# Kernel tuning notes

Hardware: AMD Instinct MI355X
Metric: run time of the kernel (lower is better)

The kernel has to match this reference:

```python
import jax, jax.numpy as jnp
import numpy as np

N = 50000   # nodes
E = 600000  # edges (avg degree 12)
D = 128     # feature dim (input_dim == output_dim for residual)
G = 8       # graphs in batch
EPS = 1e-5


def setup_inputs() -> dict:
    key = jax.random.key(0)
    ks = jax.random.split(key, 8)
    x = jax.random.normal(ks[0], (N, D), dtype=jnp.float32)
    edge_index = jax.random.randint(ks[1], (2, E), 0, N)
    batch = jnp.sort(jax.random.randint(ks[2], (N,), 0, G))
    s = 1.0 / np.sqrt(D)
    Wl = jax.random.normal(ks[3], (D, D), dtype=jnp.float32) * s
    bl = jax.random.normal(ks[4], (D,), dtype=jnp.float32) * s
    Wr = jax.random.normal(ks[5], (D, D), dtype=jnp.float32) * s
    return {
        "x": x,
        "edge_index": edge_index,
        "batch": batch,
        "num_graphs": G,
        "Wl": Wl,
        "bl": bl,
        "Wr": Wr,
        "gn_weight": jnp.ones((D,), jnp.float32),
        "gn_bias": jnp.zeros((D,), jnp.float32),
        "mean_scale": jnp.ones((D,), jnp.float32),
    }


def reference(x, edge_index, batch, num_graphs, Wl, bl, Wr, gn_weight, gn_bias, mean_scale):
    n = x.shape[0]
    src, dst = edge_index[0], edge_index[1]

    # SAGEConv: mean-aggregate neighbor (source) features at target nodes
    ones_e = jnp.ones(src.shape[0], dtype=x.dtype)
    deg = jax.ops.segment_sum(ones_e, dst, num_segments=n)          # [N]
    agg = jax.ops.segment_sum(x[src], dst, num_segments=n)          # [N, D]
    agg = agg / jnp.maximum(deg, 1.0)[:, None]
    f = agg @ Wl.T + bl + x @ Wr.T                                  # lin_l(agg) + lin_r(x)

    # exact (erf) GELU, as torch F.gelu default
    f = jax.nn.gelu(f, approximate=False)

    # GraphNorm: per-graph statistics with learnable mean_scale
    ones_n = jnp.ones(n, dtype=x.dtype)
    cnt = jax.ops.segment_sum(ones_n, batch, num_segments=num_graphs)[:, None]  # [G,1]
    mean = jax.ops.segment_sum(f, batch, num_segments=num_graphs) / cnt         # [G,D]
    out = f - mean_scale * mean[batch]
    var = jax.ops.segment_sum(out * out, batch, num_segments=num_graphs) / cnt  # [G,D]
    out = out / jnp.sqrt(var[batch] + EPS) * gn_weight + gn_bias

    # dropout is identity in eval mode; residual add
    return out + x
```

## Files before the change

### kernel.cpp

```cpp
#include <hip/hip_runtime.h>

#define D 128
#define NGRAPH 8
#define EPS 1e-5f
#define CAP 48

typedef __attribute__((ext_vector_type(4))) float f32x4;
typedef __attribute__((ext_vector_type(8))) short s16x8;

__device__ __forceinline__ unsigned short f2bf(float f) {
    unsigned int u = __float_as_uint(f);
    u += 0x7fffu + ((u >> 16) & 1u);
    return (unsigned short)(u >> 16);
}
__device__ __forceinline__ float blo(unsigned int u) { return __uint_as_float(u << 16); }
__device__ __forceinline__ float bhi(unsigned int u) { return __uint_as_float(u & 0xffff0000u); }

__global__ __launch_bounds__(256) void prep_fill_kernel(
    const float* __restrict__ Wl, const float* __restrict__ Wr,
    unsigned short* __restrict__ Bsw,
    const float* __restrict__ x, unsigned int* __restrict__ xb,
    const int* __restrict__ batch, int* __restrict__ bnd,
    const int* __restrict__ ei, int* __restrict__ cnt, int* __restrict__ adj,
    int N, int E, int Npad, int fillB)
{
    int b = blockIdx.x;
    if (b < 128) {
        int t = b * 256 + threadIdx.x;
        int j    = t & 7;
        int ln   = (t >> 3) & 63;
        int ks   = (t >> 9) & 7;
        int tile = t >> 12;
        int k = ks * 32 + (ln >> 4) * 8 + j;
        int d = tile * 16 + (ln & 15);
        float v = (k < 128) ? Wl[(size_t)d * 128 + k] : Wr[(size_t)d * 128 + (k - 128)];
        Bsw[t] = f2bf(v);
    } else if (b == 128) {
        int g = threadIdx.x;
        if (g <= NGRAPH) {
            int lo = 0, hi = N;
            while (lo < hi) {
                int mid = (lo + hi) >> 1;
                if (batch[mid] < g) lo = mid + 1; else hi = mid;
            }
            bnd[g] = lo;
        }
    } else if (b < 129 + fillB) {
        int e = (b - 129) * 256 + threadIdx.x;
        if (e < E) {
            int dst = ei[E + e];
            int pos = atomicAdd(&cnt[dst], 1);
            if (pos < CAP) adj[(size_t)dst * CAP + pos] = ei[e];
        }
    } else {
        int iu = (b - 129 - fillB) * 256 + threadIdx.x;
        if (iu < N * 32) {
            float4 p = *(const float4*)(x + (size_t)iu * 4);
            uint2 o;
            o.x = (unsigned int)f2bf(p.x) | ((unsigned int)f2bf(p.y) << 16);
            o.y = (unsigned int)f2bf(p.z) | ((unsigned int)f2bf(p.w) << 16);
            *(uint2*)(xb + (size_t)iu * 2) = o;
        } else if (iu < Npad * 32) {
            *(uint2*)(xb + (size_t)iu * 2) = make_uint2(0u, 0u);
        }
    }
}

__global__ __launch_bounds__(256) void aggregate_kernel(
    const unsigned int* __restrict__ xb, const int* __restrict__ cnt,
    const int* __restrict__ adj, unsigned int* __restrict__ Aag, int N, int Npad)
{
    int n = blockIdx.x * 4 + (threadIdx.x >> 6);
    int lane = threadIdx.x & 63;
    if (n >= Npad) return;
    if (n >= N) { Aag[(size_t)n * 64 + lane] = 0u; return; }
    int deg = cnt[n];
    int lim = deg < CAP ? deg : CAP;
    int v = (lane < lim) ? adj[(size_t)n * CAP + lane] : 0;
    float a0 = 0.0f, a1 = 0.0f;
    int i = 0;
    for (; i + 8 <= lim; i += 8) {
        int nb[8];
#pragma unroll
        for (int k = 0; k < 8; ++k) nb[k] = __shfl(v, i + k, 64);
        unsigned int u[8];
#pragma unroll
        for (int k = 0; k < 8; ++k) u[k] = xb[(size_t)nb[k] * 64 + lane];
#pragma unroll
        for (int k = 0; k < 8; ++k) { a0 += blo(u[k]); a1 += bhi(u[k]); }
    }
    for (; i < lim; ++i) {
        int nb = __shfl(v, i, 64);
        unsigned int u = xb[(size_t)nb * 64 + lane];
        a0 += blo(u); a1 += bhi(u);
    }
    float inv = 1.0f / (float)(deg > 0 ? deg : 1);
    Aag[(size_t)n * 64 + lane] =
        (unsigned int)f2bf(a0 * inv) | ((unsigned int)f2bf(a1 * inv) << 16);
}

template<int COOP>
__global__ __launch_bounds__(256, 4) void fused_kernel(
    const unsigned short* __restrict__ Aag, const unsigned short* __restrict__ xb16,
    const unsigned short* __restrict__ Bsw, const float* __restrict__ bl,
    const int* __restrict__ batch, const int* __restrict__ bnd,
    const float* __restrict__ x,
    const float* __restrict__ ms, const float* __restrict__ gw,
    const float* __restrict__ gb,
    float* __restrict__ gsum, float* __restrict__ gsumsq,
    unsigned int* __restrict__ bar, float* __restrict__ fout,
    float* __restrict__ out, int N)
{
    int wave = threadIdx.x >> 6, lane = threadIdx.x & 63;
    int row0 = blockIdx.x * 64 + wave * 16;
    int m = lane & 15, quad = lane >> 4;
    int r = row0 + m;

    s16x8 afrag[8];
    const unsigned short* ab = Aag + (size_t)r * 128 + quad * 8;
#pragma unroll
    for (int ks = 0; ks < 4; ++ks) afrag[ks] = *(const s16x8*)(ab + ks * 32);
    const unsigned short* xp = xb16 + (size_t)r * 128 + quad * 8;
#pragma unroll
    for (int ks = 0; ks < 4; ++ks) afrag[4 + ks] = *(const s16x8*)(xp + ks * 32);

    int nbase = row0;
    bool uni = (nbase + 15 < N) && (batch[nbase] == batch[nbase + 15]);
    int gu = (nbase < N) ? batch[nbase] : 0;

    float val[8][4];
#pragma unroll
    for (int tile = 0; tile < 8; ++tile) {
        f32x4 acc = {0.0f, 0.0f, 0.0f, 0.0f};
        const s16x8* bptr = (const s16x8*)Bsw + (size_t)(tile * 8) * 64 + lane;
#pragma unroll
        for (int ks = 0; ks < 8; ++ks)
            acc = __builtin_amdgcn_mfma_f32_16x16x32_bf16(afrag[ks], bptr[(size_t)ks * 64], acc, 0, 0, 0);
        int d = tile * 16 + m;
        float bias = bl[d];
        float sm = 0.0f, sq = 0.0f;
#pragma unroll
        for (int rr = 0; rr < 4; ++rr) {
            int node = nbase + quad * 4 + rr;
            float v = acc[rr] + bias;
            float g = 0.5f * v * (1.0f + erff(v * 0.70710678118654752f));
            val[tile][rr] = g;
            if (node < N) {
                if (uni) { sm += g; sq += g * g; }
                else {
                    int gg = batch[node];
                    unsafeAtomicAdd(&gsum[gg * D + d], g);
                    unsafeAtomicAdd(&gsumsq[gg * D + d], g * g);
                }
            }
        }
        if (uni) {
            sm += __shfl_xor(sm, 16, 64); sm += __shfl_xor(sm, 32, 64);
            sq += __shfl_xor(sq, 16, 64); sq += __shfl_xor(sq, 32, 64);
            if (quad == 0) {
                unsafeAtomicAdd(&gsum[gu * D + d], sm);
                unsafeAtomicAdd(&gsumsq[gu * D + d], sq);
            }
        }
    }

    if constexpr (!COOP) {
#pragma unroll
        for (int tile = 0; tile < 8; ++tile) {
            int d = tile * 16 + m;
#pragma unroll
            for (int rr = 0; rr < 4; ++rr) {
                int node = nbase + quad * 4 + rr;
                if (node < N) fout[(size_t)node * D + d] = val[tile][rr];
            }
        }
        return;
    }

    __syncthreads();
    if (threadIdx.x == 0) {
        __hip_atomic_fetch_add(bar, 1u, __ATOMIC_ACQ_REL, __HIP_MEMORY_SCOPE_AGENT);
        unsigned long long t0 = __builtin_amdgcn_s_memrealtime();
        while (__hip_atomic_load(bar, __ATOMIC_RELAXED, __HIP_MEMORY_SCOPE_AGENT) < gridDim.x) {
            __builtin_amdgcn_s_sleep(10);
            if (__builtin_amdgcn_s_memrealtime() - t0 > 5000000ull) break;
        }
    }
    __syncthreads();

    int node0 = nbase + quad * 4;
    if (node0 < N) {
        int last = (node0 + 3 < N - 1) ? node0 + 3 : N - 1;
        int g0 = batch[node0];
        int gL = batch[last];
        if (g0 == gL) {
            int c = bnd[g0 + 1] - bnd[g0];
            float invc = 1.0f / (float)(c > 0 ? c : 1);
#pragma unroll
            for (int tile = 0; tile < 8; ++tile) {
                int d = tile * 16 + m;
                float s1 = __hip_atomic_load(&gsum[g0 * D + d], __ATOMIC_RELAXED, __HIP_MEMORY_SCOPE_AGENT);
                float s2 = __hip_atomic_load(&gsumsq[g0 * D + d], __ATOMIC_RELAXED, __HIP_MEMORY_SCOPE_AGENT);
                float mu = s1 * invc, q = s2 * invc, a = ms[d] * mu;
                float sc = rsqrtf(q - 2.0f * a * mu + a * a + EPS);
                float gwv = gw[d], gbv = gb[d];
#pragma unroll
                for (int rr = 0; rr < 4; ++rr) {
                    int node = node0 + rr;
                    if (node < N)
                        out[(size_t)node * D + d] =
                            (val[tile][rr] - a) * sc * gwv + gbv + x[(size_t)node * D + d];
                }
            }
        } else {
#pragma unroll
            for (int rr = 0; rr < 4; ++rr) {
                int node = node0 + rr;
                if (node >= N) continue;
                int g = batch[node];
                int c = bnd[g + 1] - bnd[g];
                float invc = 1.0f / (float)(c > 0 ? c : 1);
#pragma unroll
                for (int tile = 0; tile < 8; ++tile) {
                    int d = tile * 16 + m;
                    float s1 = __hip_atomic_load(&gsum[g * D + d], __ATOMIC_RELAXED, __HIP_MEMORY_SCOPE_AGENT);
                    float s2 = __hip_atomic_load(&gsumsq[g * D + d], __ATOMIC_RELAXED, __HIP_MEMORY_SCOPE_AGENT);
                    float mu = s1 * invc, q = s2 * invc, a = ms[d] * mu;
                    float sc = rsqrtf(q - 2.0f * a * mu + a * a + EPS);
                    out[(size_t)node * D + d] =
                        (val[tile][rr] - a) * sc * gw[d] + gb[d] + x[(size_t)node * D + d];
                }
            }
        }
    }
}

__global__ __launch_bounds__(256) void final_kernel(
    const float* __restrict__ f, const float* __restrict__ x,
    const int* __restrict__ batch, const int* __restrict__ bnd,
    const float* __restrict__ gsum, const float* __restrict__ gsumsq,
    const float* __restrict__ ms,
    const float* __restrict__ gw, const float* __restrict__ gb,
    float* __restrict__ out, int N)
{
    int t = blockIdx.x * 256 + threadIdx.x;
    if (t >= N * (D / 4)) return;
    int n  = t >> 5;
    int d0 = (t & 31) * 4;
    int g  = batch[n];
    int c  = bnd[g + 1] - bnd[g];
    float invc = 1.0f / (float)(c > 0 ? c : 1);
    size_t row = (size_t)n * D + d0;
    float4 fv = *(const float4*)(f + row);
    float4 xv = *(const float4*)(x + row);
    float4 s1 = *(const float4*)(gsum + g * D + d0);
    float4 s2 = *(const float4*)(gsumsq + g * D + d0);
    float4 msv = *(const float4*)(ms + d0);
    float4 gwv = *(const float4*)(gw + d0);
    float4 gbv = *(const float4*)(gb + d0);
    float4 o;
    {
        float mu = s1.x * invc, q = s2.x * invc, a = msv.x * mu;
        float sc = rsqrtf(q - 2.0f * a * mu + a * a + EPS);
        o.x = (fv.x - a) * sc * gwv.x + gbv.x + xv.x;
    }
    {
        float mu = s1.y * invc, q = s2.y * invc, a = msv.y * mu;
        float sc = rsqrtf(q - 2.0f * a * mu + a * a + EPS);
        o.y = (fv.y - a) * sc * gwv.y + gbv.y + xv.y;
    }
    {
        float mu = s1.z * invc, q = s2.z * invc, a = msv.z * mu;
        float sc = rsqrtf(q - 2.0f * a * mu + a * a + EPS);
        o.z = (fv.z - a) * sc * gwv.z + gbv.z + xv.z;
    }
    {
        float mu = s1.w * invc, q = s2.w * invc, a = msv.w * mu;
        float sc = rsqrtf(q - 2.0f * a * mu + a * a + EPS);
        o.w = (fv.w - a) * sc * gwv.w + gbv.w + xv.w;
    }
    *(float4*)(out + row) = o;
}

extern "C" void kernel_launch(void* const* d_in, const int* in_sizes, int n_in,
                              void* d_out, int out_size, void* d_ws, size_t ws_size,
                              hipStream_t stream)
{
    const float* x     = (const float*)d_in[0];
    const int*   ei    = (const int*)d_in[1];
    const int*   batch = (const int*)d_in[2];
    const float* Wl = (const float*)d_in[4];
    const float* bl = (const float*)d_in[5];
    const float* Wr = (const float*)d_in[6];
    const float* gw = (const float*)d_in[7];
    const float* gb = (const float*)d_in[8];
    const float* ms = (const float*)d_in[9];
    float* out = (float*)d_out;

    int N = in_sizes[0] / D;
    int E = in_sizes[1] / 2;
    int NBLK = (N + 63) / 64;
    int Npad = NBLK * 64;

    float*          fout = (float*)d_ws;
    unsigned int*   xb   = (unsigned int*)(fout + (size_t)Npad * D);
    unsigned short* Bsw  = (unsigned short*)(xb + (size_t)Npad * 64);
    float* gsum   = (float*)(Bsw + 32768);
    float* gsumsq = gsum + NGRAPH * D;
    unsigned int* bar = (unsigned int*)(gsumsq + NGRAPH * D);
    int*   cnt    = (int*)(bar + 4);
    int*   bnd    = cnt + N;
    int*   adj    = bnd + (NGRAPH + 1);
    unsigned int* Aag = (unsigned int*)(adj + (size_t)N * CAP);

    hipMemsetAsync(gsum, 0,
                   (2 * NGRAPH * D) * sizeof(float) + 4 * sizeof(unsigned int)
                   + (size_t)N * sizeof(int), stream);

    int fillB = (E + 255) / 256;
    int xbB   = (Npad * 32 + 255) / 256;
    prep_fill_kernel<<<129 + fillB + xbB, 256, 0, stream>>>(
        Wl, Wr, Bsw, x, xb, batch, bnd, ei, cnt, adj, N, E, Npad, fillB);

    aggregate_kernel<<<Npad / 4, 256, 0, stream>>>(xb, cnt, adj, Aag, N, Npad);

    int occ = 0, ncu = 0, dev = 0;
    bool coop = false;
    if (hipOccupancyMaxActiveBlocksPerMultiprocessor(&occ, fused_kernel<1>, 256, 0) == hipSuccess) {
        if (hipGetDevice(&dev) != hipSuccess) dev = 0;
        if (hipDeviceGetAttribute(&ncu, hipDeviceAttributeMultiprocessorCount, dev) != hipSuccess || ncu <= 0)
            ncu = 256;
        coop = ((long long)occ * (long long)ncu >= (long long)NBLK);
    }

    if (coop) {
        fused_kernel<1><<<NBLK, 256, 0, stream>>>(
            (const unsigned short*)Aag, (const unsigned short*)xb, Bsw, bl,
            batch, bnd, x, ms, gw, gb, gsum, gsumsq, bar, fout, out, N);
    } else {
        fused_kernel<0><<<NBLK, 256, 0, stream>>>(
            (const unsigned short*)Aag, (const unsigned short*)xb, Bsw, bl,
            batch, bnd, x, ms, gw, gb, gsum, gsumsq, bar, fout, out, N);
        int threads = N * (D / 4);
        final_kernel<<<(threads + 255) / 256, 256, 0, stream>>>(
            fout, x, batch, bnd, gsum, gsumsq, ms, gw, gb, out, N);
    }
}
```

Before: 203.7 us.

## Gather neighbors from fp8 copy and split output columns across waves

```diff
diff --git a/kernel.cpp b/kernel.cpp
--- a/kernel.cpp
+++ b/kernel.cpp
@@ -6,6 +6,7 @@
 #define CAP 48
 
 typedef __attribute__((ext_vector_type(4))) float f32x4;
+typedef __attribute__((ext_vector_type(2))) float f32x2;
 typedef __attribute__((ext_vector_type(8))) short s16x8;
 
 __device__ __forceinline__ unsigned short f2bf(float f) {
@@ -20,6 +21,7 @@
     const float* __restrict__ Wl, const float* __restrict__ Wr,
     unsigned short* __restrict__ Bsw,
     const float* __restrict__ x, unsigned int* __restrict__ xb,
+    unsigned int* __restrict__ xf8,
     const int* __restrict__ batch, int* __restrict__ bnd,
     const int* __restrict__ ei, int* __restrict__ cnt, int* __restrict__ adj,
     int N, int E, int Npad, int fillB)
@@ -54,20 +56,27 @@
         }
     } else {
         int iu = (b - 129 - fillB) * 256 + threadIdx.x;
-        if (iu < N * 32) {
-            float4 p = *(const float4*)(x + (size_t)iu * 4);
-            uint2 o;
-            o.x = (unsigned int)f2bf(p.x) | ((unsigned int)f2bf(p.y) << 16);
-            o.y = (unsigned int)f2bf(p.z) | ((unsigned int)f2bf(p.w) << 16);
-            *(uint2*)(xb + (size_t)iu * 2) = o;
-        } else if (iu < Npad * 32) {
-            *(uint2*)(xb + (size_t)iu * 2) = make_uint2(0u, 0u);
+        if (iu < Npad * 32) {
+            int n = iu >> 5, slot = iu & 31;
+            if (iu < N * 32) {
+                float4 p = *(const float4*)(x + (size_t)iu * 4);
+                uint2 o;
+                o.x = (unsigned int)f2bf(p.x) | ((unsigned int)f2bf(p.y) << 16);
+                o.y = (unsigned int)f2bf(p.z) | ((unsigned int)f2bf(p.w) << 16);
+                *(uint2*)(xb + (size_t)iu * 2) = o;
+                int u8 = __builtin_amdgcn_cvt_pk_fp8_f32(p.x, p.y, 0, false);
+                u8     = __builtin_amdgcn_cvt_pk_fp8_f32(p.z, p.w, u8, true);
+                xf8[(size_t)n * 32 + slot] = (unsigned int)u8;
+            } else {
+                *(uint2*)(xb + (size_t)iu * 2) = make_uint2(0u, 0u);
+                xf8[(size_t)n * 32 + slot] = 0u;
+            }
         }
     }
 }
 
 __global__ __launch_bounds__(256) void aggregate_kernel(
-    const unsigned int* __restrict__ xb, const int* __restrict__ cnt,
+    const unsigned short* __restrict__ xf8, const int* __restrict__ cnt,
     const int* __restrict__ adj, unsigned int* __restrict__ Aag, int N, int Npad)
 {
     int n = blockIdx.x * 4 + (threadIdx.x >> 6);
@@ -83,16 +92,20 @@
         int nb[8];
 #pragma unroll
         for (int k = 0; k < 8; ++k) nb[k] = __shfl(v, i + k, 64);
-        unsigned int u[8];
-#pragma unroll
-        for (int k = 0; k < 8; ++k) u[k] = xb[(size_t)nb[k] * 64 + lane];
-#pragma unroll
-        for (int k = 0; k < 8; ++k) { a0 += blo(u[k]); a1 += bhi(u[k]); }
+        unsigned short u[8];
+#pragma unroll
+        for (int k = 0; k < 8; ++k) u[k] = xf8[(size_t)nb[k] * 64 + lane];
+#pragma unroll
+        for (int k = 0; k < 8; ++k) {
+            f32x2 d2 = __builtin_amdgcn_cvt_pk_f32_fp8((int)(unsigned int)u[k], false);
+            a0 += d2[0]; a1 += d2[1];
+        }
     }
     for (; i < lim; ++i) {
         int nb = __shfl(v, i, 64);
-        unsigned int u = xb[(size_t)nb * 64 + lane];
-        a0 += blo(u); a1 += bhi(u);
+        f32x2 d2 = __builtin_amdgcn_cvt_pk_f32_fp8(
+            (int)(unsigned int)xf8[(size_t)nb * 64 + lane], false);
+        a0 += d2[0]; a1 += d2[1];
     }
     float inv = 1.0f / (float)(deg > 0 ? deg : 1);
     Aag[(size_t)n * 64 + lane] =
@@ -100,7 +113,7 @@
 }
 
 template<int COOP>
-__global__ __launch_bounds__(256, 4) void fused_kernel(
+__global__ __launch_bounds__(256, 8) void fused_kernel(
     const unsigned short* __restrict__ Aag, const unsigned short* __restrict__ xb16,
     const unsigned short* __restrict__ Bsw, const float* __restrict__ bl,
     const int* __restrict__ batch, const int* __restrict__ bnd,
@@ -112,7 +125,8 @@
     float* __restrict__ out, int N)
 {
     int wave = threadIdx.x >> 6, lane = threadIdx.x & 63;
-    int row0 = blockIdx.x * 64 + wave * 16;
+    int row0 = blockIdx.x * 32 + (wave >> 1) * 16;
+    int th = wave & 1;
     int m = lane & 15, quad = lane >> 4;
     int r = row0 + m;
 
@@ -128,9 +142,10 @@
     bool uni = (nbase + 15 < N) && (batch[nbase] == batch[nbase + 15]);
     int gu = (nbase < N) ? batch[nbase] : 0;
 
-    float val[8][4];
-#pragma unroll
-    for (int tile = 0; tile < 8; ++tile) {
+    float val[4][4];
+#pragma unroll
+    for (int t = 0; t < 4; ++t) {
+        int tile = th * 4 + t;
         f32x4 acc = {0.0f, 0.0f, 0.0f, 0.0f};
         const s16x8* bptr = (const s16x8*)Bsw + (size_t)(tile * 8) * 64 + lane;
 #pragma unroll
@@ -144,7 +159,7 @@
             int node = nbase + quad * 4 + rr;
             float v = acc[rr] + bias;
             float g = 0.5f * v * (1.0f + erff(v * 0.70710678118654752f));
-            val[tile][rr] = g;
+            val[t][rr] = g;
             if (node < N) {
                 if (uni) { sm += g; sq += g * g; }
                 else {
@@ -166,12 +181,12 @@
 
     if constexpr (!COOP) {
 #pragma unroll
-        for (int tile = 0; tile < 8; ++tile) {
-            int d = tile * 16 + m;
+        for (int t = 0; t < 4; ++t) {
+            int d = (th * 4 + t) * 16 + m;
 #pragma unroll
             for (int rr = 0; rr < 4; ++rr) {
                 int node = nbase + quad * 4 + rr;
-                if (node < N) fout[(size_t)node * D + d] = val[tile][rr];
+                if (node < N) fout[(size_t)node * D + d] = val[t][rr];
             }
         }
         return;
@@ -197,8 +212,8 @@
             int c = bnd[g0 + 1] - bnd[g0];
             float invc = 1.0f / (float)(c > 0 ? c : 1);
 #pragma unroll
-            for (int tile = 0; tile < 8; ++tile) {
-                int d = tile * 16 + m;
+            for (int t = 0; t < 4; ++t) {
+                int d = (th * 4 + t) * 16 + m;
                 float s1 = __hip_atomic_load(&gsum[g0 * D + d], __ATOMIC_RELAXED, __HIP_MEMORY_SCOPE_AGENT);
                 float s2 = __hip_atomic_load(&gsumsq[g0 * D + d], __ATOMIC_RELAXED, __HIP_MEMORY_SCOPE_AGENT);
                 float mu = s1 * invc, q = s2 * invc, a = ms[d] * mu;
@@ -209,7 +224,7 @@
                     int node = node0 + rr;
                     if (node < N)
                         out[(size_t)node * D + d] =
-                            (val[tile][rr] - a) * sc * gwv + gbv + x[(size_t)node * D + d];
+                            (val[t][rr] - a) * sc * gwv + gbv + x[(size_t)node * D + d];
                 }
             }
         } else {
@@ -221,14 +236,14 @@
                 int c = bnd[g + 1] - bnd[g];
                 float invc = 1.0f / (float)(c > 0 ? c : 1);
 #pragma unroll
-                for (int tile = 0; tile < 8; ++tile) {
-                    int d = tile * 16 + m;
+                for (int t = 0; t < 4; ++t) {
+                    int d = (th * 4 + t) * 16 + m;
                     float s1 = __hip_atomic_load(&gsum[g * D + d], __ATOMIC_RELAXED, __HIP_MEMORY_SCOPE_AGENT);
                     float s2 = __hip_atomic_load(&gsumsq[g * D + d], __ATOMIC_RELAXED, __HIP_MEMORY_SCOPE_AGENT);
                     float mu = s1 * invc, q = s2 * invc, a = ms[d] * mu;
                     float sc = rsqrtf(q - 2.0f * a * mu + a * a + EPS);
                     out[(size_t)node * D + d] =
-                        (val[tile][rr] - a) * sc * gw[d] + gb[d] + x[(size_t)node * D + d];
+                        (val[t][rr] - a) * sc * gw[d] + gb[d] + x[(size_t)node * D + d];
                 }
             }
         }
@@ -301,8 +316,10 @@
     int E = in_sizes[1] / 2;
     int NBLK = (N + 63) / 64;
     int Npad = NBLK * 64;
+    int NB32 = Npad / 32;
 
     float*          fout = (float*)d_ws;
+    unsigned int*   xf8  = (unsigned int*)fout;
     unsigned int*   xb   = (unsigned int*)(fout + (size_t)Npad * D);
     unsigned short* Bsw  = (unsigned short*)(xb + (size_t)Npad * 64);
     float* gsum   = (float*)(Bsw + 32768);
@@ -320,9 +337,10 @@
     int fillB = (E + 255) / 256;
     int xbB   = (Npad * 32 + 255) / 256;
     prep_fill_kernel<<<129 + fillB + xbB, 256, 0, stream>>>(
-        Wl, Wr, Bsw, x, xb, batch, bnd, ei, cnt, adj, N, E, Npad, fillB);
-
-    aggregate_kernel<<<Npad / 4, 256, 0, stream>>>(xb, cnt, adj, Aag, N, Npad);
+        Wl, Wr, Bsw, x, xb, xf8, batch, bnd, ei, cnt, adj, N, E, Npad, fillB);
+
+    aggregate_kernel<<<Npad / 4, 256, 0, stream>>>(
+        (const unsigned short*)xf8, cnt, adj, Aag, N, Npad);
 
     int occ = 0, ncu = 0, dev = 0;
     bool coop = false;
@@ -330,15 +348,15 @@
         if (hipGetDevice(&dev) != hipSuccess) dev = 0;
         if (hipDeviceGetAttribute(&ncu, hipDeviceAttributeMultiprocessorCount, dev) != hipSuccess || ncu <= 0)
             ncu = 256;
-        coop = ((long long)occ * (long long)ncu >= (long long)NBLK);
+        coop = ((long long)occ * (long long)ncu >= (long long)NB32);
     }
 
     if (coop) {
-        fused_kernel<1><<<NBLK, 256, 0, stream>>>(
+        fused_kernel<1><<<NB32, 256, 0, stream>>>(
             (const unsigned short*)Aag, (const unsigned short*)xb, Bsw, bl,
             batch, bnd, x, ms, gw, gb, gsum, gsumsq, bar, fout, out, N);
     } else {
-        fused_kernel<0><<<NBLK, 256, 0, stream>>>(
+        fused_kernel<0><<<NB32, 256, 0, stream>>>(
             (const unsigned short*)Aag, (const unsigned short*)xb, Bsw, bl,
             batch, bnd, x, ms, gw, gb, gsum, gsumsq, bar, fout, out, N);
         int threads = N * (D / 4);
```

New measurement: 204.3 us. About the same (+0.3%).
